# Kernel tuning notes

Hardware: AMD Instinct MI355X
Metric: run time of the kernel (lower is better)

The kernel has to match this reference:

```python
import jax, jax.numpy as jnp
import numpy as np

K = 32
D = 256


def setup_inputs() -> dict:
    key = jax.random.key(0)
    k1, k2, kW, kV, kb = jax.random.split(key, 5)
    B, L1, L2 = 16, 256, 256
    x1 = jax.random.normal(k1, (B, L1, D), dtype=jnp.float32)
    x2 = jax.random.normal(k2, (B, L2, D), dtype=jnp.float32)
    # kaiming_uniform-style init bounds
    bound_W = np.sqrt(6.0 / ((1 + 5) * D))  # fan_in = d, a=sqrt(5)
    W = jax.random.uniform(kW, (K, D, D), minval=-bound_W, maxval=bound_W, dtype=jnp.float32)
    bound_V = np.sqrt(6.0 / ((1 + 5) * 2 * D))
    V = jax.random.uniform(kV, (K, 2 * D), minval=-bound_V, maxval=bound_V, dtype=jnp.float32)
    bound_b = 1.0 / np.sqrt(2 * D)
    b = jax.random.uniform(kb, (K,), minval=-bound_b, maxval=bound_b, dtype=jnp.float32)
    return {"x1": x1, "x2": x2, "W": W, "V": V, "b": b}


def reference(x1, x2, W, V, b):
    # x1: [B,L1,d], x2: [B,L2,d], W: [k,d,d], V: [k,2d], b: [k]
    d = x1.shape[-1]
    # bilinear term: (x1 W) x2^T per output channel k -> [B,k,L1,L2]
    temp = jnp.einsum('bld,kde->bkle', x1, W)            # [B,k,L1,d]
    bilinear_out = jnp.einsum('bkle,bme->bklm', temp, x2)  # [B,k,L1,L2]
    # linear term: V @ concat(x1,x2) = V1 x1 + V2 x2, broadcast-summed
    V1, V2 = V[:, :d], V[:, d:]
    lin1 = jnp.einsum('bld,kd->bkl', x1, V1)             # [B,k,L1]
    lin2 = jnp.einsum('bmd,kd->bkm', x2, V2)             # [B,k,L2]
    linear_out = lin1[:, :, :, None] + lin2[:, :, None, :] + b[None, :, None, None]
    return jax.nn.relu(bilinear_out + linear_out)
```

## Files before the change

### kernel.cpp

```cpp
#include <hip/hip_runtime.h>
#include <hip/hip_bf16.h>

typedef unsigned short u16;
typedef __bf16 bf16x8 __attribute__((ext_vector_type(8)));
typedef float f32x4 __attribute__((ext_vector_type(4)));

#define NB 16
#define NK 32
#define ND 256
#define NL 256

__device__ __forceinline__ u16 f2bf(float f) {
    __hip_bfloat16 h = __float2bfloat16(f);
    return __builtin_bit_cast(u16, h);
}

__device__ __forceinline__ void gload_lds16(const void* g, void* l) {
    __builtin_amdgcn_global_load_lds(
        (const __attribute__((address_space(1))) unsigned int*)g,
        (__attribute__((address_space(3))) unsigned int*)l, 16, 0, 0);
}


__global__ void prep_kernel(const float* __restrict__ x1, const float* __restrict__ x2,
                            const float* __restrict__ W,
                            u16* __restrict__ x1f, u16* __restrict__ x2f, u16* __restrict__ Wf) {
    int bid = blockIdx.x;
    int tid = threadIdx.x;
    const float* src; u16* dst; long f4;
    if (bid < 1024)      { src = x1; dst = x1f; f4 = (long)bid * 256 + tid; }
    else if (bid < 2048) { src = x2; dst = x2f; f4 = (long)(bid - 1024) * 256 + tid; }
    else                 { src = W;  dst = Wf;  f4 = (long)(bid - 2048) * 256 + tid; }
    long idx = f4 << 2;
    int mat = (int)(idx >> 16);
    int r = (int)((idx >> 8) & 255);
    int c = (int)(idx & 255);
    float4 v = ((const float4*)src)[f4];
    ushort4 o;
    o.x = f2bf(v.x); o.y = f2bf(v.y); o.z = f2bf(v.z); o.w = f2bf(v.w);
    int rt = r >> 4, ct = c >> 5;
    int lane = (r & 15) | (((c >> 3) & 3) << 4);
    long off = ((long)mat << 16) + (((rt << 3) + ct) << 9) + (lane << 3) + (c & 7);
    *(ushort4*)(dst + off) = o;
}

__launch_bounds__(512, 6)
__global__ void ntn_main(const u16* __restrict__ x1f, const u16* __restrict__ x2f,
                         const u16* __restrict__ Wf,
                         const float* __restrict__ V, const float* __restrict__ bb,
                         float* __restrict__ out) {
    __shared__ __align__(16) char ldsRaw[32768];
    __shared__ float rlin[64];

    int bid = blockIdx.x;
    int xcd   = bid & 7;
    int j     = bid >> 3;
    int slot  = j >> 7;
    int inner = j & 127;
    int st    = (slot << 3) | xcd;
    int kg = st >> 2, bg = st & 3;
    int k  = (kg << 3) | (inner >> 4);
    int b  = (bg << 2) | ((inner >> 2) & 3);
    int mq = inner & 3;

    int tid  = threadIdx.x;
    int lane = tid & 63;
    int wid  = tid >> 6;
    int lrow = lane & 15;
    int j4   = (lane >> 4) << 2;

    {
        const char* src = (const char*)(x2f + ((long)b << 16) + ((long)mq << 14));
#pragma unroll
        for (int it = 0; it < 4; ++it) {
            int chunk = (it << 3) + wid;
            gload_lds16(src + (chunk << 10) + (lane << 4), ldsRaw + (chunk << 10));
        }
    }

    float bk = bb[k];
    f32x4 acc[4][2];
    const f32x4 fz = {0.f, 0.f, 0.f, 0.f};
#pragma unroll
    for (int i = 0; i < 4; ++i) { acc[i][0] = fz; acc[i][1] = fz; }

    __syncthreads();

    {
        int ml = tid >> 3;
        int et = tid & 7;
        const float* v2p = V + ((long)k << 9) + 256 + (et << 5);
        float sum = 0.f;
#pragma unroll
        for (int eg = 0; eg < 4; ++eg) {
            int lp = (ml & 15) | (eg << 4);
            bf16x8 xv = *(const bf16x8*)(ldsRaw + ((((ml >> 4) << 3) + et) << 10) + (lp << 4));
            float4 va = *(const float4*)(v2p + (eg << 3));
            float4 vb = *(const float4*)(v2p + (eg << 3) + 4);
            sum += (float)xv[0] * va.x + (float)xv[1] * va.y + (float)xv[2] * va.z + (float)xv[3] * va.w
                 + (float)xv[4] * vb.x + (float)xv[5] * vb.y + (float)xv[6] * vb.z + (float)xv[7] * vb.w;
        }
        sum += __shfl_xor(sum, 1);
        sum += __shfl_xor(sum, 2);
        sum += __shfl_xor(sum, 4);
        if ((tid & 7) == 0) rlin[ml] = sum + bk;
    }

    {
        int wrA = wid >> 1;
        int wcA = wid & 1;
        const u16* wp = Wf + ((long)k << 16);
#pragma unroll
        for (int et = 0; et < 8; ++et) {
            bf16x8 af[4], bfr[2];
#pragma unroll
            for (int lt = 0; lt < 4; ++lt)
                af[lt] = *(const bf16x8*)(wp + (((((wrA << 2) + lt) << 3) + et) << 9) + (lane << 3));
#pragma unroll
            for (int nt = 0; nt < 2; ++nt)
                bfr[nt] = *(const bf16x8*)(ldsRaw + ((((((wcA << 1) + nt) << 3) + et) << 10) + (lane << 4)));
#pragma unroll
            for (int nt = 0; nt < 2; ++nt)
#pragma unroll
                for (int lt = 0; lt < 4; ++lt)
                    acc[lt][nt] = __builtin_amdgcn_mfma_f32_16x16x32_bf16(af[lt], bfr[nt], acc[lt][nt], 0, 0, 0);
        }
    }
    __syncthreads();

    {
        int wrA = wid >> 1;
        int wcA = wid & 1;
        const float* v1base = V + ((long)k << 9);
#pragma unroll
        for (int lt = 0; lt < 4; ++lt) {
            int d0 = (wrA << 6) + (lt << 4) + j4;
            float4 v1q = *(const float4*)(v1base + d0);
#pragma unroll
            for (int nt = 0; nt < 2; ++nt) {
                int m = (wcA << 5) + (nt << 4) + lrow;
                ushort4 pk;
                pk.x = f2bf(acc[lt][nt][0] + v1q.x);
                pk.y = f2bf(acc[lt][nt][1] + v1q.y);
                pk.z = f2bf(acc[lt][nt][2] + v1q.z);
                pk.w = f2bf(acc[lt][nt][3] + v1q.w);
                *(ushort4*)(ldsRaw + (m << 9) + ((d0 << 1) ^ ((m & 7) << 4))) = pk;
            }
        }
    }
    __syncthreads();

#pragma unroll
    for (int i = 0; i < 4; ++i) { acc[i][0] = fz; acc[i][1] = fz; }

    {
        const u16* x1p = x1f + ((long)b << 16);
        int lk8 = (lane >> 4) << 3;
#pragma unroll
        for (int dt = 0; dt < 8; ++dt) {
            int d = (dt << 5) + lk8;
            bf16x8 am[4], xl[2];
#pragma unroll
            for (int mt = 0; mt < 4; ++mt) {
                int m = (mt << 4) + lrow;
                am[mt] = *(const bf16x8*)(ldsRaw + (m << 9) + ((d << 1) ^ ((m & 7) << 4)));
            }
#pragma unroll
            for (int lt = 0; lt < 2; ++lt)
                xl[lt] = *(const bf16x8*)(x1p + (((((wid << 1) + lt) << 3) + dt) << 9) + (lane << 3));
#pragma unroll
            for (int lt = 0; lt < 2; ++lt)
#pragma unroll
                for (int mt = 0; mt < 4; ++mt)
                    acc[mt][lt] = __builtin_amdgcn_mfma_f32_16x16x32_bf16(am[mt], xl[lt], acc[mt][lt], 0, 0, 0);
        }
    }
    __syncthreads();

    {
        float* outp = out + (((long)(b * NK + k)) << 16) + (mq << 6);

#pragma unroll
        for (int c = 0; c < 2; ++c) {
            if ((wid >> 2) == c) {
#pragma unroll
                for (int mt = 0; mt < 4; ++mt) {
                    int mcol = (mt << 4) + j4;
                    float4 rv = *(const float4*)(rlin + mcol);
#pragma unroll
                    for (int lt = 0; lt < 2; ++lt) {
                        int row = ((wid & 3) << 5) + (lt << 4) + lrow;
                        f32x4 v;
                        v[0] = acc[mt][lt][0] + rv.x;
                        v[1] = acc[mt][lt][1] + rv.y;
                        v[2] = acc[mt][lt][2] + rv.z;
                        v[3] = acc[mt][lt][3] + rv.w;
                        v[0] = v[0] > 0.f ? v[0] : 0.f;
                        v[1] = v[1] > 0.f ? v[1] : 0.f;
                        v[2] = v[2] > 0.f ? v[2] : 0.f;
                        v[3] = v[3] > 0.f ? v[3] : 0.f;
                        *(f32x4*)(ldsRaw + (row << 8) + ((mcol << 2) ^ ((row & 7) << 4))) = v;
                    }
                }
            }
            __syncthreads();
#pragma unroll
            for (int it = 0; it < 4; ++it) {
                int g = (it << 9) + tid;
                int row = g >> 4;
                int c4  = g & 15;
                f32x4 v = *(const f32x4*)(ldsRaw + (row << 8) + ((c4 << 4) ^ ((row & 7) << 4)));
                *(f32x4*)(outp + ((long)((c << 7) + row) << 8) + (c4 << 2)) = v;
            }
            if (c == 0) __syncthreads();
        }
    }
}

extern "C" void kernel_launch(void* const* d_in, const int* in_sizes, int n_in,
                              void* d_out, int out_size, void* d_ws, size_t ws_size,
                              hipStream_t stream) {
    const float* x1 = (const float*)d_in[0];
    const float* x2 = (const float*)d_in[1];
    const float* W  = (const float*)d_in[2];
    const float* V  = (const float*)d_in[3];
    const float* bb = (const float*)d_in[4];
    float* out = (float*)d_out;

    char* ws = (char*)d_ws;
    u16*   x1f  = (u16*)(ws);
    u16*   x2f  = (u16*)(ws + (2l << 20));
    u16*   Wf   = (u16*)(ws + (4l << 20));

    hipLaunchKernelGGL(prep_kernel, dim3(4096), dim3(256), 0, stream,
                       x1, x2, W, x1f, x2f, Wf);
    hipLaunchKernelGGL(ntn_main, dim3(2048), dim3(512), 0, stream,
                       x1f, x2f, Wf, V, bb, out);
}
```

Baseline: 72.59 us.

## Tile over L1 rows and transpose W in prep to write contiguous output rows

```diff
diff --git a/kernel.cpp b/kernel.cpp
--- a/kernel.cpp
+++ b/kernel.cpp
@@ -2,6 +2,7 @@
 #include <hip/hip_bf16.h>
 
 typedef unsigned short u16;
+typedef unsigned short ushort8v __attribute__((ext_vector_type(8)));
 typedef __bf16 bf16x8 __attribute__((ext_vector_type(8)));
 typedef float f32x4 __attribute__((ext_vector_type(4)));
 
@@ -24,33 +25,62 @@
 
 __global__ void prep_kernel(const float* __restrict__ x1, const float* __restrict__ x2,
                             const float* __restrict__ W,
-                            u16* __restrict__ x1f, u16* __restrict__ x2f, u16* __restrict__ Wf) {
+                            u16* __restrict__ x1f, u16* __restrict__ x2f, u16* __restrict__ Wtf) {
+    __shared__ float xs[32 * 260];
     int bid = blockIdx.x;
     int tid = threadIdx.x;
-    const float* src; u16* dst; long f4;
-    if (bid < 1024)      { src = x1; dst = x1f; f4 = (long)bid * 256 + tid; }
-    else if (bid < 2048) { src = x2; dst = x2f; f4 = (long)(bid - 1024) * 256 + tid; }
-    else                 { src = W;  dst = Wf;  f4 = (long)(bid - 2048) * 256 + tid; }
-    long idx = f4 << 2;
-    int mat = (int)(idx >> 16);
-    int r = (int)((idx >> 8) & 255);
-    int c = (int)(idx & 255);
-    float4 v = ((const float4*)src)[f4];
-    ushort4 o;
-    o.x = f2bf(v.x); o.y = f2bf(v.y); o.z = f2bf(v.z); o.w = f2bf(v.w);
-    int rt = r >> 4, ct = c >> 5;
-    int lane = (r & 15) | (((c >> 3) & 3) << 4);
-    long off = ((long)mat << 16) + (((rt << 3) + ct) << 9) + (lane << 3) + (c & 7);
-    *(ushort4*)(dst + off) = o;
-}
-
-__launch_bounds__(512, 6)
+    if (bid < 2048) {
+        const float* src; u16* dst; long f4;
+        if (bid < 1024) { src = x1; dst = x1f; f4 = (long)bid * 256 + tid; }
+        else            { src = x2; dst = x2f; f4 = (long)(bid - 1024) * 256 + tid; }
+        long idx = f4 << 2;
+        int mat = (int)(idx >> 16);
+        int r = (int)((idx >> 8) & 255);
+        int c = (int)(idx & 255);
+        float4 v = ((const float4*)src)[f4];
+        ushort4 o;
+        o.x = f2bf(v.x); o.y = f2bf(v.y); o.z = f2bf(v.z); o.w = f2bf(v.w);
+        int rt = r >> 4, ct = c >> 5;
+        int lane = (r & 15) | (((c >> 3) & 3) << 4);
+        long off = ((long)mat << 16) + (((rt << 3) + ct) << 9) + (lane << 3) + (c & 7);
+        *(ushort4*)(dst + off) = o;
+        return;
+    }
+    int wb = bid - 2048;
+    int k  = wb >> 3;
+    int dg = wb & 7;
+    const float* wsrc = W + ((long)k << 16) + ((long)dg << 13);
+#pragma unroll
+    for (int it = 0; it < 8; ++it) {
+        int ch = (it << 8) + tid;
+        int row = ch >> 6;
+        int col4 = ch & 63;
+        float4 v = *(const float4*)(wsrc + (row << 8) + (col4 << 2));
+        *(float4*)(xs + row * 260 + (col4 << 2)) = v;
+    }
+    __syncthreads();
+    int e = tid;
+    int rt = e >> 4;
+    u16* wdst = Wtf + ((long)k << 16) + ((long)((rt << 3) + dg) << 9);
+#pragma unroll
+    for (int g = 0; g < 4; ++g) {
+        ushort8v pk;
+#pragma unroll
+        for (int q = 0; q < 8; ++q)
+            pk[q] = f2bf(xs[((g << 3) + q) * 260 + e]);
+        *(ushort8v*)(wdst + (((e & 15) | (g << 4)) << 3)) = pk;
+    }
+}
+
+__launch_bounds__(512, 4)
 __global__ void ntn_main(const u16* __restrict__ x1f, const u16* __restrict__ x2f,
-                         const u16* __restrict__ Wf,
+                         const u16* __restrict__ Wtf,
                          const float* __restrict__ V, const float* __restrict__ bb,
                          float* __restrict__ out) {
-    __shared__ __align__(16) char ldsRaw[32768];
-    __shared__ float rlin[64];
+    __shared__ __align__(16) char ldsA[32768];
+    __shared__ __align__(16) char ldsT[32768];
+    __shared__ float r1[64];
+    __shared__ float r2[256];
 
     int bid = blockIdx.x;
     int xcd   = bid & 7;
@@ -61,145 +91,160 @@
     int kg = st >> 2, bg = st & 3;
     int k  = (kg << 3) | (inner >> 4);
     int b  = (bg << 2) | ((inner >> 2) & 3);
-    int mq = inner & 3;
+    int lq = inner & 3;
 
     int tid  = threadIdx.x;
     int lane = tid & 63;
     int wid  = tid >> 6;
+    int wm = wid >> 1;
+    int wl = wid & 1;
     int lrow = lane & 15;
     int j4   = (lane >> 4) << 2;
-
-    {
-        const char* src = (const char*)(x2f + ((long)b << 16) + ((long)mq << 14));
+    int lk8  = (lane >> 4) << 3;
+
+    {
+        const char* src = (const char*)(x1f + ((long)b << 16) + ((long)lq << 14));
 #pragma unroll
         for (int it = 0; it < 4; ++it) {
             int chunk = (it << 3) + wid;
-            gload_lds16(src + (chunk << 10) + (lane << 4), ldsRaw + (chunk << 10));
-        }
-    }
-
-    float bk = bb[k];
+            gload_lds16(src + (chunk << 10) + (lane << 4), ldsA + (chunk << 10));
+        }
+    }
+    __syncthreads();
+
+    {
+        int ll = tid >> 3;
+        int et8 = tid & 7;
+        const float* v1p = V + ((long)k << 9) + (et8 << 5);
+        float s = 0.f;
+#pragma unroll
+        for (int eg = 0; eg < 4; ++eg) {
+            int lp = (ll & 15) | (eg << 4);
+            bf16x8 xv = *(const bf16x8*)(ldsA + ((((ll >> 4) << 3) + et8) << 10) + (lp << 4));
+            float4 va = *(const float4*)(v1p + (eg << 3));
+            float4 vb = *(const float4*)(v1p + (eg << 3) + 4);
+            s += (float)xv[0] * va.x + (float)xv[1] * va.y + (float)xv[2] * va.z + (float)xv[3] * va.w
+               + (float)xv[4] * vb.x + (float)xv[5] * vb.y + (float)xv[6] * vb.z + (float)xv[7] * vb.w;
+        }
+        s += __shfl_xor(s, 1);
+        s += __shfl_xor(s, 2);
+        s += __shfl_xor(s, 4);
+        if ((tid & 7) == 0) r1[ll] = s;
+    }
+
+    {
+        int mm = tid >> 1;
+        int eh = tid & 1;
+        const u16* x2p = x2f + ((long)b << 16);
+        const float* v2p = V + ((long)k << 9) + 256;
+        float s = 0.f;
+#pragma unroll
+        for (int t4 = 0; t4 < 4; ++t4) {
+            int et = (eh << 2) + t4;
+#pragma unroll
+            for (int eg = 0; eg < 4; ++eg) {
+                int lp = (mm & 15) | (eg << 4);
+                bf16x8 xv = *(const bf16x8*)(x2p + ((((mm >> 4) << 3) + et) << 9) + (lp << 3));
+                const float* vv = v2p + (et << 5) + (eg << 3);
+                float4 va = *(const float4*)(vv);
+                float4 vb = *(const float4*)(vv + 4);
+                s += (float)xv[0] * va.x + (float)xv[1] * va.y + (float)xv[2] * va.z + (float)xv[3] * va.w
+                   + (float)xv[4] * vb.x + (float)xv[5] * vb.y + (float)xv[6] * vb.z + (float)xv[7] * vb.w;
+            }
+        }
+        s += __shfl_xor(s, 1);
+        if (eh == 0) r2[mm] = s + bb[k];
+    }
+
+    const f32x4 fz = {0.f, 0.f, 0.f, 0.f};
     f32x4 acc[4][2];
-    const f32x4 fz = {0.f, 0.f, 0.f, 0.f};
-#pragma unroll
-    for (int i = 0; i < 4; ++i) { acc[i][0] = fz; acc[i][1] = fz; }
-
-    __syncthreads();
-
-    {
-        int ml = tid >> 3;
-        int et = tid & 7;
-        const float* v2p = V + ((long)k << 9) + 256 + (et << 5);
-        float sum = 0.f;
-#pragma unroll
-        for (int eg = 0; eg < 4; ++eg) {
-            int lp = (ml & 15) | (eg << 4);
-            bf16x8 xv = *(const bf16x8*)(ldsRaw + ((((ml >> 4) << 3) + et) << 10) + (lp << 4));
-            float4 va = *(const float4*)(v2p + (eg << 3));
-            float4 vb = *(const float4*)(v2p + (eg << 3) + 4);
-            sum += (float)xv[0] * va.x + (float)xv[1] * va.y + (float)xv[2] * va.z + (float)xv[3] * va.w
-                 + (float)xv[4] * vb.x + (float)xv[5] * vb.y + (float)xv[6] * vb.z + (float)xv[7] * vb.w;
-        }
-        sum += __shfl_xor(sum, 1);
-        sum += __shfl_xor(sum, 2);
-        sum += __shfl_xor(sum, 4);
-        if ((tid & 7) == 0) rlin[ml] = sum + bk;
-    }
-
-    {
-        int wrA = wid >> 1;
-        int wcA = wid & 1;
-        const u16* wp = Wf + ((long)k << 16);
+#pragma unroll
+    for (int q = 0; q < 4; ++q) { acc[q][0] = fz; acc[q][1] = fz; }
+
+    {
+        const u16* wtp = Wtf + ((long)k << 16);
+#pragma unroll
+        for (int dt = 0; dt < 8; ++dt) {
+            bf16x8 af[4], bfl[2];
+#pragma unroll
+            for (int q = 0; q < 4; ++q)
+                af[q] = *(const bf16x8*)(wtp + (((((wm << 2) + q) << 3) + dt) << 9) + (lane << 3));
+#pragma unroll
+            for (int p = 0; p < 2; ++p)
+                bfl[p] = *(const bf16x8*)(ldsA + ((((((wl << 1) + p) << 3) + dt) << 10) + (lane << 4)));
+#pragma unroll
+            for (int p = 0; p < 2; ++p)
+#pragma unroll
+                for (int q = 0; q < 4; ++q)
+                    acc[q][p] = __builtin_amdgcn_mfma_f32_16x16x32_bf16(af[q], bfl[p], acc[q][p], 0, 0, 0);
+        }
+    }
+    __syncthreads();
+
+#pragma unroll
+    for (int q = 0; q < 4; ++q) {
+        int e0 = (wm << 6) + (q << 4) + j4;
+#pragma unroll
+        for (int p = 0; p < 2; ++p) {
+            int l = (wl << 5) + (p << 4) + lrow;
+            ushort4 pk;
+            pk.x = f2bf(acc[q][p][0]);
+            pk.y = f2bf(acc[q][p][1]);
+            pk.z = f2bf(acc[q][p][2]);
+            pk.w = f2bf(acc[q][p][3]);
+            *(ushort4*)(ldsT + (l << 9) + ((e0 << 1) ^ ((l & 7) << 4))) = pk;
+        }
+    }
+    __syncthreads();
+
+#pragma unroll
+    for (int q = 0; q < 4; ++q) { acc[q][0] = fz; acc[q][1] = fz; }
+
+    {
+        const u16* x2p = x2f + ((long)b << 16);
 #pragma unroll
         for (int et = 0; et < 8; ++et) {
-            bf16x8 af[4], bfr[2];
-#pragma unroll
-            for (int lt = 0; lt < 4; ++lt)
-                af[lt] = *(const bf16x8*)(wp + (((((wrA << 2) + lt) << 3) + et) << 9) + (lane << 3));
-#pragma unroll
-            for (int nt = 0; nt < 2; ++nt)
-                bfr[nt] = *(const bf16x8*)(ldsRaw + ((((((wcA << 1) + nt) << 3) + et) << 10) + (lane << 4)));
-#pragma unroll
-            for (int nt = 0; nt < 2; ++nt)
-#pragma unroll
-                for (int lt = 0; lt < 4; ++lt)
-                    acc[lt][nt] = __builtin_amdgcn_mfma_f32_16x16x32_bf16(af[lt], bfr[nt], acc[lt][nt], 0, 0, 0);
-        }
-    }
-    __syncthreads();
-
-    {
-        int wrA = wid >> 1;
-        int wcA = wid & 1;
-        const float* v1base = V + ((long)k << 9);
-#pragma unroll
-        for (int lt = 0; lt < 4; ++lt) {
-            int d0 = (wrA << 6) + (lt << 4) + j4;
-            float4 v1q = *(const float4*)(v1base + d0);
-#pragma unroll
-            for (int nt = 0; nt < 2; ++nt) {
-                int m = (wcA << 5) + (nt << 4) + lrow;
-                ushort4 pk;
-                pk.x = f2bf(acc[lt][nt][0] + v1q.x);
-                pk.y = f2bf(acc[lt][nt][1] + v1q.y);
-                pk.z = f2bf(acc[lt][nt][2] + v1q.z);
-                pk.w = f2bf(acc[lt][nt][3] + v1q.w);
-                *(ushort4*)(ldsRaw + (m << 9) + ((d0 << 1) ^ ((m & 7) << 4))) = pk;
-            }
-        }
-    }
-    __syncthreads();
-
-#pragma unroll
-    for (int i = 0; i < 4; ++i) { acc[i][0] = fz; acc[i][1] = fz; }
-
-    {
-        const u16* x1p = x1f + ((long)b << 16);
-        int lk8 = (lane >> 4) << 3;
-#pragma unroll
-        for (int dt = 0; dt < 8; ++dt) {
-            int d = (dt << 5) + lk8;
-            bf16x8 am[4], xl[2];
-#pragma unroll
-            for (int mt = 0; mt < 4; ++mt) {
-                int m = (mt << 4) + lrow;
-                am[mt] = *(const bf16x8*)(ldsRaw + (m << 9) + ((d << 1) ^ ((m & 7) << 4)));
-            }
-#pragma unroll
-            for (int lt = 0; lt < 2; ++lt)
-                xl[lt] = *(const bf16x8*)(x1p + (((((wid << 1) + lt) << 3) + dt) << 9) + (lane << 3));
-#pragma unroll
-            for (int lt = 0; lt < 2; ++lt)
-#pragma unroll
-                for (int mt = 0; mt < 4; ++mt)
-                    acc[mt][lt] = __builtin_amdgcn_mfma_f32_16x16x32_bf16(am[mt], xl[lt], acc[mt][lt], 0, 0, 0);
-        }
-    }
-    __syncthreads();
-
-    {
-        float* outp = out + (((long)(b * NK + k)) << 16) + (mq << 6);
-
+            int e = (et << 5) + lk8;
+            bf16x8 am[4], tf[2];
+#pragma unroll
+            for (int q = 0; q < 4; ++q)
+                am[q] = *(const bf16x8*)(x2p + (((((wm << 2) + q) << 3) + et) << 9) + (lane << 3));
+#pragma unroll
+            for (int p = 0; p < 2; ++p) {
+                int l = (wl << 5) + (p << 4) + lrow;
+                tf[p] = *(const bf16x8*)(ldsT + (l << 9) + ((e << 1) ^ ((l & 7) << 4)));
+            }
+#pragma unroll
+            for (int p = 0; p < 2; ++p)
+#pragma unroll
+                for (int q = 0; q < 4; ++q)
+                    acc[q][p] = __builtin_amdgcn_mfma_f32_16x16x32_bf16(am[q], tf[p], acc[q][p], 0, 0, 0);
+        }
+    }
+
+    {
+        float* outp = out + (((long)(b * NK + k)) << 16) + ((long)(lq << 6) << 8);
 #pragma unroll
         for (int c = 0; c < 2; ++c) {
-            if ((wid >> 2) == c) {
-#pragma unroll
-                for (int mt = 0; mt < 4; ++mt) {
-                    int mcol = (mt << 4) + j4;
-                    float4 rv = *(const float4*)(rlin + mcol);
-#pragma unroll
-                    for (int lt = 0; lt < 2; ++lt) {
-                        int row = ((wid & 3) << 5) + (lt << 4) + lrow;
+            if (wl == c) {
+#pragma unroll
+                for (int q = 0; q < 4; ++q) {
+                    int m0 = (wm << 6) + (q << 4) + j4;
+                    float4 rv = *(const float4*)(r2 + m0);
+#pragma unroll
+                    for (int p = 0; p < 2; ++p) {
+                        int row = (p << 4) + lrow;
+                        float rb = r1[(c << 5) + row];
                         f32x4 v;
-                        v[0] = acc[mt][lt][0] + rv.x;
-                        v[1] = acc[mt][lt][1] + rv.y;
-                        v[2] = acc[mt][lt][2] + rv.z;
-                        v[3] = acc[mt][lt][3] + rv.w;
+                        v[0] = acc[q][p][0] + rb + rv.x;
+                        v[1] = acc[q][p][1] + rb + rv.y;
+                        v[2] = acc[q][p][2] + rb + rv.z;
+                        v[3] = acc[q][p][3] + rb + rv.w;
                         v[0] = v[0] > 0.f ? v[0] : 0.f;
                         v[1] = v[1] > 0.f ? v[1] : 0.f;
                         v[2] = v[2] > 0.f ? v[2] : 0.f;
                         v[3] = v[3] > 0.f ? v[3] : 0.f;
-                        *(f32x4*)(ldsRaw + (row << 8) + ((mcol << 2) ^ ((row & 7) << 4))) = v;
+                        *(f32x4*)(ldsA + (row << 10) + ((m0 << 2) ^ ((row & 7) << 4))) = v;
                     }
                 }
             }
@@ -207,10 +252,10 @@
 #pragma unroll
             for (int it = 0; it < 4; ++it) {
                 int g = (it << 9) + tid;
-                int row = g >> 4;
-                int c4  = g & 15;
-                f32x4 v = *(const f32x4*)(ldsRaw + (row << 8) + ((c4 << 4) ^ ((row & 7) << 4)));
-                *(f32x4*)(outp + ((long)((c << 7) + row) << 8) + (c4 << 2)) = v;
+                int row = g >> 6;
+                int c4  = g & 63;
+                f32x4 v = *(const f32x4*)(ldsA + (row << 10) + ((c4 << 4) ^ ((row & 7) << 4)));
+                *(f32x4*)(outp + ((long)((c << 5) + row) << 8) + (c4 << 2)) = v;
             }
             if (c == 0) __syncthreads();
         }
@@ -230,10 +275,10 @@
     char* ws = (char*)d_ws;
     u16*   x1f  = (u16*)(ws);
     u16*   x2f  = (u16*)(ws + (2l << 20));
-    u16*   Wf   = (u16*)(ws + (4l << 20));
-
-    hipLaunchKernelGGL(prep_kernel, dim3(4096), dim3(256), 0, stream,
-                       x1, x2, W, x1f, x2f, Wf);
+    u16*   Wtf  = (u16*)(ws + (4l << 20));
+
+    hipLaunchKernelGGL(prep_kernel, dim3(2304), dim3(256), 0, stream,
+                       x1, x2, W, x1f, x2f, Wtf);
     hipLaunchKernelGGL(ntn_main, dim3(2048), dim3(512), 0, stream,
-                       x1f, x2f, Wf, V, bb, out);
-}
+                       x1f, x2f, Wtf, V, bb, out);
+}
```

Result: slower. 112.8 us (+55.4%).
